# Optimization experiments

Measured on AMD Instinct MI355X. Metric: run time of the kernel, lower is better.

## Reference

```python
import jax, jax.numpy as jnp
import numpy as np

N = 100000   # nodes
E = 1600000  # directed edges
D_IN, D_HID, D_OUT, N_CLS = 128, 256, 128, 10
EPS = 1e-5


def gcn_conv(x, W, b, src, dst, n):
    # PyG GCNConv: h = XW, add self loops, sym-normalize, scatter-add to dst, + bias
    h = x @ W
    loop = jnp.arange(n)
    src_f = jnp.concatenate([src, loop])
    dst_f = jnp.concatenate([dst, loop])
    deg = jax.ops.segment_sum(jnp.ones(src_f.shape[0], h.dtype), dst_f, num_segments=n)
    dinv = jnp.where(deg > 0, jax.lax.rsqrt(deg), jnp.zeros_like(deg))
    norm = dinv[src_f] * dinv[dst_f]                    # [E+N]
    out = jax.ops.segment_sum(h[src_f] * norm[:, None], dst_f, num_segments=n)
    return out + b


def batchnorm(x, gamma, beta):
    # training-mode BatchNorm1d (batch statistics, biased variance)
    mu = x.mean(0)
    var = x.var(0)
    return gamma * (x - mu) * jax.lax.rsqrt(var + EPS) + beta


def setup_inputs() -> dict:
    key = jax.random.key(0)
    ks = jax.random.split(key, 12)
    x = jax.random.normal(ks[0], (N, D_IN), jnp.float32)
    edge_index = jax.random.randint(ks[1], (2, E), 0, N, dtype=jnp.int64)
    def lin(k, fi, fo):
        s = 1.0 / np.sqrt(fi)
        return jax.random.uniform(k, (fi, fo), jnp.float32, -s, s)
    return {
        "x": x, "edge_index": edge_index,
        "W1": lin(ks[2], D_IN, D_HID), "b1": jnp.zeros(D_HID, jnp.float32),
        "g1": jnp.ones(D_HID, jnp.float32), "beta1": jnp.zeros(D_HID, jnp.float32),
        "W2": lin(ks[3], D_HID, D_HID), "b2": jnp.zeros(D_HID, jnp.float32),
        "g2": jnp.ones(D_HID, jnp.float32), "beta2": jnp.zeros(D_HID, jnp.float32),
        "W3": lin(ks[4], D_HID, D_OUT), "b3": jnp.zeros(D_OUT, jnp.float32),
        "g3": jnp.ones(D_OUT, jnp.float32), "beta3": jnp.zeros(D_OUT, jnp.float32),
        "Wout": lin(ks[5], D_OUT, N_CLS), "bout": jnp.zeros(N_CLS, jnp.float32),
    }


def reference(x, edge_index, W1, b1, g1, beta1, W2, b2, g2, beta2,
              W3, b3, g3, beta3, Wout, bout):
    src, dst = edge_index[0], edge_index[1]
    h = jax.nn.relu(batchnorm(gcn_conv(x, W1, b1, src, dst, N), g1, beta1))
    h = jax.nn.relu(batchnorm(gcn_conv(h, W2, b2, src, dst, N), g2, beta2))
    h = jax.nn.relu(batchnorm(gcn_conv(h, W3, b3, src, dst, N), g3, beta3))
    return h @ Wout + bout
```

## Files before the change

kernel.cpp:

```cpp
#include <hip/hip_runtime.h>
#include <hip/hip_fp16.h>
#include <cstdint>
#include <cstddef>

#define EPS_BN 1e-5f
#define NSLICE 16

static inline int cdiv(int a, int b) { return (a + b - 1) / b; }

using half8   = __attribute__((ext_vector_type(8))) _Float16;
using floatx4 = __attribute__((ext_vector_type(4))) float;

__device__ __forceinline__ float atomAddF(float* p, float v) {
    return unsafeAtomicAdd(p, v);
}


__global__ __launch_bounds__(256) void k_hist(const int* __restrict__ dst, int E,
                                              int NBLK, int NBUCK, int* __restrict__ H) {
    __shared__ int h[256];
    int t = threadIdx.x;
    h[t] = 0;
    __syncthreads();
    int base = blockIdx.x * 4096;
#pragma unroll
    for (int j = 0; j < 16; ++j) {
        int e = base + j * 256 + t;
        if (e < E) atomicAdd(&h[dst[e] >> 9], 1);
    }
    __syncthreads();
    if (t < NBUCK) H[t * NBLK + blockIdx.x] = h[t];
}

__global__ __launch_bounds__(256) void k_scan_reduce(const int* __restrict__ in, int m,
                                                     int* __restrict__ bsum) {
    int base = blockIdx.x * 1024;
    int t = threadIdx.x;
    int s = 0;
#pragma unroll
    for (int i = 0; i < 4; ++i) {
        int idx = base + t * 4 + i;
        if (idx < m) s += in[idx];
    }
    __shared__ int sm[256];
    sm[t] = s;
    __syncthreads();
    for (int off = 128; off > 0; off >>= 1) {
        if (t < off) sm[t] += sm[t + off];
        __syncthreads();
    }
    if (t == 0) bsum[blockIdx.x] = sm[0];
}

__global__ void k_scan_bsum(int* __restrict__ bsum, int nb) {
    if (threadIdx.x == 0 && blockIdx.x == 0) {
        int acc = 0;
        for (int i = 0; i < nb; ++i) { int v = bsum[i]; bsum[i] = acc; acc += v; }
    }
}

__global__ __launch_bounds__(256) void k_scan_final(const int* __restrict__ in, int m,
                                                    const int* __restrict__ bsum,
                                                    int* __restrict__ outS) {
    int base = blockIdx.x * 1024;
    int t = threadIdx.x;
    int v[4];
    int s = 0;
#pragma unroll
    for (int i = 0; i < 4; ++i) {
        int idx = base + t * 4 + i;
        v[i] = (idx < m) ? in[idx] : 0;
        s += v[i];
    }
    __shared__ int sm[256];
    sm[t] = s;
    __syncthreads();
    for (int off = 1; off < 256; off <<= 1) {
        int x = (t >= off) ? sm[t - off] : 0;
        __syncthreads();
        sm[t] += x;
        __syncthreads();
    }
    int excl = sm[t] - s + bsum[blockIdx.x];
#pragma unroll
    for (int i = 0; i < 4; ++i) {
        int idx = base + t * 4 + i;
        if (idx < m) { outS[idx] = excl; excl += v[i]; }
    }
}

__global__ __launch_bounds__(256) void k_bucket(const int* __restrict__ src,
                                                const int* __restrict__ dst, int E,
                                                int NBLK, int NBUCK,
                                                const int* __restrict__ S,
                                                unsigned* __restrict__ pairs) {
    __shared__ int cur[256];
    int t = threadIdx.x;
    if (t < NBUCK) cur[t] = S[t * NBLK + blockIdx.x];
    __syncthreads();
    int base = blockIdx.x * 4096;
#pragma unroll
    for (int j = 0; j < 16; ++j) {
        int e = base + j * 256 + t;
        if (e < E) {
            unsigned s = (unsigned)src[e];
            unsigned d = (unsigned)dst[e];
            int p = atomicAdd(&cur[d >> 9], 1);
            pairs[p] = ((d & 511u) << 17) | s;
        }
    }
}

__global__ __launch_bounds__(256) void k_build(const unsigned* __restrict__ pairs,
                                               const int* __restrict__ S,
                                               int NBLK, int NBUCK, int n, int E,
                                               int* __restrict__ endoff,
                                               float* __restrict__ dinv,
                                               int* __restrict__ csr) {
    int b = blockIdx.x;
    int nbase = b << 9;
    int bstart = S[b * NBLK];
    int bend = (b == NBUCK - 1) ? E : S[(b + 1) * NBLK];
    int t = threadIdx.x;
    __shared__ int sdeg[512];
    __shared__ int scur[512];
    __shared__ int stmp[256];
    sdeg[t] = 0; sdeg[t + 256] = 0;
    __syncthreads();
    for (int e = bstart + t; e < bend; e += 256)
        atomicAdd(&sdeg[pairs[e] >> 17], 1);
    __syncthreads();
    int d0 = sdeg[2 * t], d1 = sdeg[2 * t + 1];
    int ps = d0 + d1;
    stmp[t] = ps;
    __syncthreads();
    for (int off = 1; off < 256; off <<= 1) {
        int x = (t >= off) ? stmp[t - off] : 0;
        __syncthreads();
        stmp[t] += x;
        __syncthreads();
    }
    int c0 = bstart + stmp[t] - ps;
    int c1 = c0 + d0;
    scur[2 * t] = c0;
    scur[2 * t + 1] = c1;
    int v0 = nbase + 2 * t, v1 = v0 + 1;
    if (v0 < n) { endoff[v0] = c1;      dinv[v0] = rsqrtf((float)(d0 + 1)); }
    if (v1 < n) { endoff[v1] = c1 + d1; dinv[v1] = rsqrtf((float)(d1 + 1)); }
    __syncthreads();
    for (int e = bstart + t; e < bend; e += 256) {
        unsigned p = pairs[e];
        int pos = atomicAdd(&scur[p >> 17], 1);
        csr[pos] = (int)(p & 0x1FFFFu);
    }
}

__global__ __launch_bounds__(256) void k_prep(const float* __restrict__ x,
                                              const float* __restrict__ dinv,
                                              const float* __restrict__ W1,
                                              const float* __restrict__ W2,
                                              const float* __restrict__ W3,
                                              __half* __restrict__ xh,
                                              __half* __restrict__ Wt1,
                                              __half* __restrict__ Wt2,
                                              __half* __restrict__ Wt3,
                                              float* __restrict__ stats, int n) {
    int idx = blockIdx.x * 256 + threadIdx.x;
    int nx = n * 16;
    if (idx < nx) {
        int row = idx >> 4;
        float dv = dinv[row];
        const float4* p = (const float4*)x + (size_t)idx * 2;
        float4 a = p[0], b = p[1];
        uint4 o; __half2* oh = (__half2*)&o;
        oh[0] = __floats2half2_rn(a.x * dv, a.y * dv);
        oh[1] = __floats2half2_rn(a.z * dv, a.w * dv);
        oh[2] = __floats2half2_rn(b.x * dv, b.y * dv);
        oh[3] = __floats2half2_rn(b.z * dv, b.w * dv);
        ((uint4*)xh)[idx] = o;
        return;
    }
    int r = idx - nx;
    if (r < 32768) {
        int k = r >> 8, c = r & 255;
        Wt1[c * 128 + k] = __float2half(W1[r]);
    } else if (r < 98304) {
        int r2 = r - 32768;
        int k = r2 >> 8, c = r2 & 255;
        Wt2[c * 256 + k] = __float2half(W2[r2]);
    } else if (r < 131072) {
        int r2 = r - 98304;
        int k = r2 >> 7, c = r2 & 127;
        Wt3[c * 256 + k] = __float2half(W3[r2]);
    } else if (r < 131072 + NSLICE * 256 * 6) {
        stats[r - 131072] = 0.f;
    }
}

__device__ __forceinline__ void acc8(float* acc, uint4 d) {
    const __half2* h = (const __half2*)&d;
#pragma unroll
    for (int j = 0; j < 4; ++j) {
        float2 f = __half22float2(h[j]);
        acc[2 * j] += f.x; acc[2 * j + 1] += f.y;
    }
}

template<int D, bool STATS>
__global__ __launch_bounds__(256) void k_gather_h(const int* __restrict__ csr,
                                                  const int* __restrict__ endoff,
                                                  const __half* __restrict__ P,
                                                  const float* __restrict__ dinv,
                                                  __half* __restrict__ S, int n,
                                                  float* __restrict__ sums,
                                                  float* __restrict__ sqs) {
    constexpr int LPN = D / 8;
    constexpr int NPB = 256 / LPN;
    __shared__ float red[STATS ? 2048 : 1];
    int t = threadIdx.x;
    int lane = t % LPN;
    int sub = t / LPN;
    float sacc[8] = {}, sqacc[8] = {};
    for (int vb = blockIdx.x * NPB; vb < n; vb += gridDim.x * NPB) {
        int v = vb + sub;
        if (v >= n) continue;
        int beg = (v == 0) ? 0 : endoff[v - 1];
        int end = endoff[v];
        float acc[8];
        {
            uint4 d = *((const uint4*)(P + (size_t)v * D) + lane);
            const __half2* h = (const __half2*)&d;
#pragma unroll
            for (int j = 0; j < 4; ++j) {
                float2 f = __half22float2(h[j]);
                acc[2 * j] = f.x; acc[2 * j + 1] = f.y;
            }
        }
        int i = beg;
        int rem = (end - beg) & 7;
        if (rem & 4) {
            uint4 dd[4];
#pragma unroll
            for (int u = 0; u < 4; ++u)
                dd[u] = *((const uint4*)(P + (size_t)csr[i + u] * D) + lane);
#pragma unroll
            for (int u = 0; u < 4; ++u) acc8(acc, dd[u]);
            i += 4;
        }
        if (rem & 2) {
            uint4 d0 = *((const uint4*)(P + (size_t)csr[i] * D) + lane);
            uint4 d1 = *((const uint4*)(P + (size_t)csr[i + 1] * D) + lane);
            acc8(acc, d0); acc8(acc, d1);
            i += 2;
        }
        if (rem & 1) {
            uint4 d0 = *((const uint4*)(P + (size_t)csr[i] * D) + lane);
            acc8(acc, d0);
            i += 1;
        }
        if (i < end) {
            uint4 a[8];
#pragma unroll
            for (int u = 0; u < 8; ++u)
                a[u] = *((const uint4*)(P + (size_t)csr[i + u] * D) + lane);
            for (i += 8; i < end; i += 8) {
                uint4 b[8];
#pragma unroll
                for (int u = 0; u < 8; ++u)
                    b[u] = *((const uint4*)(P + (size_t)csr[i + u] * D) + lane);
#pragma unroll
                for (int u = 0; u < 8; ++u) acc8(acc, a[u]);
#pragma unroll
                for (int u = 0; u < 8; ++u) a[u] = b[u];
            }
#pragma unroll
            for (int u = 0; u < 8; ++u) acc8(acc, a[u]);
        }
        float dv = dinv[v];
        uint4 o; __half2* oh = (__half2*)&o;
#pragma unroll
        for (int j = 0; j < 4; ++j) {
            float a0 = acc[2 * j] * dv, a1 = acc[2 * j + 1] * dv;
            oh[j] = __floats2half2_rn(a0, a1);
            if (STATS) {
                sacc[2 * j] += a0;  sqacc[2 * j] += a0 * a0;
                sacc[2 * j + 1] += a1; sqacc[2 * j + 1] += a1 * a1;
            }
        }
        *((uint4*)(S + (size_t)v * D) + lane) = o;
    }
    if (STATS) {
        int slice = blockIdx.x & (NSLICE - 1);
#pragma unroll
        for (int j = 0; j < 8; ++j) red[t * 8 + j] = sacc[j];
        __syncthreads();
        if (t < D) {
            int lc = t >> 3, j = t & 7;
            float ts = 0.f;
#pragma unroll
            for (int s = 0; s < NPB; ++s) ts += red[(s * LPN + lc) * 8 + j];
            atomAddF(&sums[slice * 256 + t], ts);
        }
        __syncthreads();
#pragma unroll
        for (int j = 0; j < 8; ++j) red[t * 8 + j] = sqacc[j];
        __syncthreads();
        if (t < D) {
            int lc = t >> 3, j = t & 7;
            float tq = 0.f;
#pragma unroll
            for (int s = 0; s < NPB; ++s) tq += red[(s * LPN + lc) * 8 + j];
            atomAddF(&sqs[slice * 256 + t], tq);
        }
    }
}

template<int K, int NC, bool SCALE, bool BNIN, bool STATS>
__global__ __launch_bounds__(256) void k_gemm_mfma(const __half* __restrict__ A,
                                                   const __half* __restrict__ Wt,
                                                   const float* __restrict__ dinv,
                                                   const float* __restrict__ isum,
                                                   const float* __restrict__ isq,
                                                   const float* __restrict__ g,
                                                   const float* __restrict__ beta,
                                                   float* __restrict__ osum,
                                                   float* __restrict__ osq,
                                                   __half* __restrict__ C, int n) {
    constexpr int LDA = 40;
    __shared__ _Float16 As[128 * LDA];
    __shared__ _Float16 Bs[128 * LDA];
    __shared__ float ssc[BNIN ? K : 1];
    __shared__ float ssh[BNIN ? K : 1];
    __shared__ float scs[STATS ? 128 : 1];
    __shared__ float scq[STATS ? 128 : 1];
    int tid = threadIdx.x;
    if (BNIN) {
        float nf = (float)n;
        for (int i = tid; i < K; i += 256) {
            float su = 0.f, sq = 0.f;
#pragma unroll
            for (int s = 0; s < NSLICE; ++s) {
                su += isum[s * 256 + i];
                sq += isq[s * 256 + i];
            }
            float mu = su / nf;
            float var = sq / nf - mu * mu;
            float sc = g[i] * rsqrtf(var + EPS_BN);
            ssc[i] = sc; ssh[i] = beta[i] - mu * sc;
        }
        __syncthreads();
    }
    int wave = tid >> 6, lane = tid & 63;
    int wr = wave >> 1, wc = wave & 1;
    int q = lane >> 4, l16 = lane & 15;
    int row0 = blockIdx.x * 128;
    int col0 = blockIdx.y * 128;
    floatx4 acc[4][4];
#pragma unroll
    for (int r = 0; r < 4; ++r)
#pragma unroll
        for (int c = 0; c < 4; ++c) acc[r][c] = (floatx4)0.0f;

    for (int k0 = 0; k0 < K; k0 += 32) {
#pragma unroll
        for (int i = 0; i < 2; ++i) {
            int s = tid + i * 256;
            int r = s >> 2, ks = s & 3;
            uint4 d = *(const uint4*)(A + (size_t)(row0 + r) * K + k0 + ks * 8);
            if (BNIN) {
                const __half2* h = (const __half2*)&d;
                uint4 o; __half2* oh = (__half2*)&o;
                int kb = k0 + ks * 8;
#pragma unroll
                for (int j = 0; j < 4; ++j) {
                    float2 f = __half22float2(h[j]);
                    float y0 = fmaxf(0.f, f.x * ssc[kb + 2 * j]     + ssh[kb + 2 * j]);
                    float y1 = fmaxf(0.f, f.y * ssc[kb + 2 * j + 1] + ssh[kb + 2 * j + 1]);
                    oh[j] = __floats2half2_rn(y0, y1);
                }
                d = o;
            }
            *(uint4*)&As[r * LDA + ks * 8] = d;
        }
#pragma unroll
        for (int i = 0; i < 2; ++i) {
            int s = tid + i * 256;
            int r = s >> 2, ks = s & 3;
            uint4 d = *(const uint4*)(Wt + (size_t)(col0 + r) * K + k0 + ks * 8);
            *(uint4*)&Bs[r * LDA + ks * 8] = d;
        }
        __syncthreads();
        half8 af[4], bf[4];
#pragma unroll
        for (int r = 0; r < 4; ++r)
            af[r] = *(const half8*)&As[(wr * 64 + r * 16 + l16) * LDA + q * 8];
#pragma unroll
        for (int c = 0; c < 4; ++c)
            bf[c] = *(const half8*)&Bs[(wc * 64 + c * 16 + l16) * LDA + q * 8];
#pragma unroll
        for (int r = 0; r < 4; ++r)
#pragma unroll
            for (int c = 0; c < 4; ++c)
                acc[r][c] = __builtin_amdgcn_mfma_f32_16x16x32_f16(af[r], bf[c], acc[r][c], 0, 0, 0);
        __syncthreads();
    }
    float colsum[4] = {};
    float colsq[4]  = {};
#pragma unroll
    for (int r = 0; r < 4; ++r) {
#pragma unroll
        for (int reg = 0; reg < 4; ++reg) {
            int grow = row0 + wr * 64 + r * 16 + q * 4 + reg;
            float sc = 1.f;
            if (SCALE) sc = (grow < n) ? dinv[grow] : 0.f;
            __half* cp = C + (size_t)grow * NC + col0 + wc * 64 + l16;
#pragma unroll
            for (int c = 0; c < 4; ++c) {
                float v = acc[r][c][reg] * sc;
                cp[c * 16] = __float2half(v);
                if (STATS && grow < n) { colsum[c] += v; colsq[c] += v * v; }
            }
        }
    }
    if (STATS) {
        if (tid < 128) { scs[tid] = 0.f; scq[tid] = 0.f; }
        __syncthreads();
#pragma unroll
        for (int c = 0; c < 4; ++c) {
            atomicAdd(&scs[wc * 64 + c * 16 + l16], colsum[c]);
            atomicAdd(&scq[wc * 64 + c * 16 + l16], colsq[c]);
        }
        __syncthreads();
        if (tid < 128) {
            int slice = blockIdx.x & (NSLICE - 1);
            atomAddF(&osum[slice * 256 + col0 + tid], scs[tid]);
            atomAddF(&osq[slice * 256 + col0 + tid], scq[tid]);
        }
    }
}

__global__ __launch_bounds__(256) void k_out(const __half* __restrict__ H,
                                             const float* __restrict__ sums,
                                             const float* __restrict__ sqs,
                                             const float* __restrict__ g,
                                             const float* __restrict__ beta,
                                             const float* __restrict__ Wout,
                                             const float* __restrict__ bout,
                                             float* __restrict__ out, int n) {
    __shared__ float Wl[128 * 10];
    __shared__ float bl[10];
    __shared__ float osc[128];
    __shared__ float osh[128];
    __shared__ float red[256 * 10];
    int tid = threadIdx.x;
    for (int i = tid; i < 1280; i += 256) Wl[i] = Wout[i];
    if (tid < 10) bl[tid] = bout[tid];
    if (tid < 128) {
        float nf = (float)n;
        float su = 0.f, sq = 0.f;
#pragma unroll
        for (int s = 0; s < NSLICE; ++s) {
            su += sums[s * 256 + tid];
            sq += sqs[s * 256 + tid];
        }
        float mu = su / nf;
        float var = sq / nf - mu * mu;
        float sc = g[tid] * rsqrtf(var + EPS_BN);
        osc[tid] = sc; osh[tid] = beta[tid] - mu * sc;
    }
    __syncthreads();
    int rl = tid >> 1;
    int h2 = tid & 1;
    int r = blockIdx.x * 128 + rl;
    float p[10] = {};
    if (r < n) {
        const __half* a = H + (size_t)r * 128 + h2 * 64;
#pragma unroll 8
        for (int k = 0; k < 64; ++k) {
            int col = h2 * 64 + k;
            float av = fmaxf(0.f, __half2float(a[k]) * osc[col] + osh[col]);
            const float* wr = Wl + col * 10;
#pragma unroll
            for (int c = 0; c < 10; ++c) p[c] += av * wr[c];
        }
    }
    float* rr = red + (size_t)tid * 10;
#pragma unroll
    for (int c = 0; c < 10; ++c) rr[c] = p[c];
    __syncthreads();
    if (h2 == 0 && r < n) {
        const float* rb = red + (size_t)tid * 10;
#pragma unroll
        for (int c = 0; c < 10; ++c) {
            out[(size_t)r * 10 + c] = rb[c] + rb[10 + c] + bl[c];
        }
    }
}

extern "C" void kernel_launch(void* const* d_in, const int* in_sizes, int n_in,
                              void* d_out, int out_size, void* d_ws, size_t ws_size,
                              hipStream_t stream) {
    const float* x    = (const float*)d_in[0];
    const int*   ei   = (const int*)d_in[1];
    const float* W1   = (const float*)d_in[2];
    const float* g1   = (const float*)d_in[4];
    const float* be1  = (const float*)d_in[5];
    const float* W2   = (const float*)d_in[6];
    const float* g2   = (const float*)d_in[8];
    const float* be2  = (const float*)d_in[9];
    const float* W3   = (const float*)d_in[10];
    const float* g3   = (const float*)d_in[12];
    const float* be3  = (const float*)d_in[13];
    const float* Wout = (const float*)d_in[14];
    const float* bout = (const float*)d_in[15];
    float* out = (float*)d_out;

    int n = in_sizes[0] / 128;
    int E = in_sizes[1] / 2;
    const int* esrc = ei;
    const int* edst = ei + E;
    int npad = cdiv(n, 128) * 128;
    int NBLK = cdiv(E, 4096);
    int NBUCK = (n + 511) >> 9;
    if (NBUCK > 256) return;
    int m = NBUCK * NBLK;
    int nb2 = cdiv(m, 1024);

    const size_t align = 256;
    auto al = [&](size_t s) { return (s + align - 1) & ~(align - 1); };
    size_t n4 = al((size_t)n * 4 + 512);

    const size_t statsLayer = (size_t)NSLICE * 256 * 2 * 4;
    const size_t statsTotal = statsLayer * 3;

    char* ws = (char*)d_ws;
    size_t o_end   = 0;
    size_t o_dinv  = o_end + n4;
    size_t o_stats = o_dinv + n4;
    size_t o_bsum  = o_stats + statsTotal;
    size_t o_H     = o_bsum + 1024;
    size_t o_Hs    = o_H + al((size_t)m * 4);
    size_t o_csr   = o_Hs + al((size_t)m * 4);
    size_t o_pairs = o_csr + al((size_t)E * 4);
    size_t o_w1    = o_pairs + al((size_t)E * 4);
    size_t o_w2    = o_w1 + al(256 * 128 * 2);
    size_t o_w3    = o_w2 + al(256 * 256 * 2);
    size_t o_A128a = o_w3 + al(128 * 256 * 2);
    size_t o_A128b = o_A128a + al((size_t)npad * 128 * 2);
    size_t o_A256a = o_A128b + al((size_t)npad * 128 * 2);
    size_t o_A256b = o_A256a + al((size_t)npad * 256 * 2);
    size_t need    = o_A256b + (size_t)npad * 256 * 2;
    if (ws_size < need) return;

    int*      endoff = (int*)(ws + o_end);
    float*    dinv   = (float*)(ws + o_dinv);
    float*    stats  = (float*)(ws + o_stats);
    float*    sums1  = stats;
    float*    sqs1   = sums1 + NSLICE * 256;
    float*    sums2  = (float*)(ws + o_stats + statsLayer);
    float*    sqs2   = sums2 + NSLICE * 256;
    float*    sums3  = (float*)(ws + o_stats + 2 * statsLayer);
    float*    sqs3   = sums3 + NSLICE * 256;
    int*      bsum   = (int*)(ws + o_bsum);
    int*      H      = (int*)(ws + o_H);
    int*      Hs     = (int*)(ws + o_Hs);
    int*      csr    = (int*)(ws + o_csr);
    unsigned* pairs  = (unsigned*)(ws + o_pairs);
    __half*   Wt1    = (__half*)(ws + o_w1);
    __half*   Wt2    = (__half*)(ws + o_w2);
    __half*   Wt3    = (__half*)(ws + o_w3);
    __half*   xh     = (__half*)(ws + o_A128a);
    __half*   S3     = (__half*)(ws + o_A128a);
    __half*   G1     = (__half*)(ws + o_A128b);
    __half*   P3     = (__half*)(ws + o_A128b);
    __half*   P1     = (__half*)(ws + o_A256a);
    __half*   S2     = (__half*)(ws + o_A256a);
    __half*   P2     = (__half*)(ws + o_A256b);

    k_hist<<<NBLK, 256, 0, stream>>>(edst, E, NBLK, NBUCK, H);
    k_scan_reduce<<<nb2, 256, 0, stream>>>(H, m, bsum);
    k_scan_bsum<<<1, 64, 0, stream>>>(bsum, nb2);
    k_scan_final<<<nb2, 256, 0, stream>>>(H, m, bsum, Hs);
    k_bucket<<<NBLK, 256, 0, stream>>>(esrc, edst, E, NBLK, NBUCK, Hs, pairs);
    k_build<<<NBUCK, 256, 0, stream>>>(pairs, Hs, NBLK, NBUCK, n, E, endoff, dinv, csr);

    int prepTotal = n * 16 + 131072 + NSLICE * 256 * 6;
    k_prep<<<cdiv(prepTotal, 256), 256, 0, stream>>>(
        x, dinv, W1, W2, W3, xh, Wt1, Wt2, Wt3, stats, n);

    k_gather_h<128, false><<<cdiv(n, 16), 256, 0, stream>>>(
        csr, endoff, xh, dinv, G1, n, nullptr, nullptr);
    k_gemm_mfma<128, 256, false, false, true><<<dim3(npad / 128, 2), 256, 0, stream>>>(
        G1, Wt1, dinv, nullptr, nullptr, nullptr, nullptr, sums1, sqs1, P1, n);

    k_gemm_mfma<256, 256, true, true, false><<<dim3(npad / 128, 2), 256, 0, stream>>>(
        P1, Wt2, dinv, sums1, sqs1, g1, be1, nullptr, nullptr, P2, n);
    k_gather_h<256, true><<<cdiv(n, 8), 256, 0, stream>>>(
        csr, endoff, P2, dinv, S2, n, sums2, sqs2);

    k_gemm_mfma<256, 128, true, true, false><<<dim3(npad / 128, 1), 256, 0, stream>>>(
        S2, Wt3, dinv, sums2, sqs2, g2, be2, nullptr, nullptr, P3, n);
    k_gather_h<128, true><<<cdiv(n, 16), 256, 0, stream>>>(
        csr, endoff, P3, dinv, S3, n, sums3, sqs3);

    k_out<<<cdiv(n, 128), 256, 0, stream>>>(S3, sums3, sqs3, g3, be3, Wout, bout, out, n);
}
```

Measured before the change: 568.5 us.

## Prefetch GEMM tiles into registers and collapse bucket scan into one kernel

The MFMA GEMM now loads the next K-slice of A and W into registers while the current slice is being multiplied, then writes them to shared memory after the compute. This overlaps global load latency with MFMA work. Separately, the three-kernel scan is replaced by a single-block scan, and histogram/bucket blocks now cover 8192 edges each, halving the histogram size. The goal is fewer launches and less preprocessing overhead. The single-block scan serializes more work per thread, and prefetching raises register pressure.

```diff
diff --git a/kernel.cpp b/kernel.cpp
--- a/kernel.cpp
+++ b/kernel.cpp
@@ -22,9 +22,9 @@
     int t = threadIdx.x;
     h[t] = 0;
     __syncthreads();
-    int base = blockIdx.x * 4096;
-#pragma unroll
-    for (int j = 0; j < 16; ++j) {
+    int base = blockIdx.x * 8192;
+#pragma unroll
+    for (int j = 0; j < 32; ++j) {
         int e = base + j * 256 + t;
         if (e < E) atomicAdd(&h[dst[e] >> 9], 1);
     }
@@ -32,47 +32,15 @@
     if (t < NBUCK) H[t * NBLK + blockIdx.x] = h[t];
 }
 
-__global__ __launch_bounds__(256) void k_scan_reduce(const int* __restrict__ in, int m,
-                                                     int* __restrict__ bsum) {
-    int base = blockIdx.x * 1024;
+__global__ __launch_bounds__(256) void k_scan_one(const int* __restrict__ in, int m,
+                                                  int* __restrict__ outS) {
+    __shared__ int sm[256];
     int t = threadIdx.x;
+    int per = (m + 255) / 256;
+    int b0 = t * per;
+    int b1 = b0 + per; if (b1 > m) b1 = m;
     int s = 0;
-#pragma unroll
-    for (int i = 0; i < 4; ++i) {
-        int idx = base + t * 4 + i;
-        if (idx < m) s += in[idx];
-    }
-    __shared__ int sm[256];
-    sm[t] = s;
-    __syncthreads();
-    for (int off = 128; off > 0; off >>= 1) {
-        if (t < off) sm[t] += sm[t + off];
-        __syncthreads();
-    }
-    if (t == 0) bsum[blockIdx.x] = sm[0];
-}
-
-__global__ void k_scan_bsum(int* __restrict__ bsum, int nb) {
-    if (threadIdx.x == 0 && blockIdx.x == 0) {
-        int acc = 0;
-        for (int i = 0; i < nb; ++i) { int v = bsum[i]; bsum[i] = acc; acc += v; }
-    }
-}
-
-__global__ __launch_bounds__(256) void k_scan_final(const int* __restrict__ in, int m,
-                                                    const int* __restrict__ bsum,
-                                                    int* __restrict__ outS) {
-    int base = blockIdx.x * 1024;
-    int t = threadIdx.x;
-    int v[4];
-    int s = 0;
-#pragma unroll
-    for (int i = 0; i < 4; ++i) {
-        int idx = base + t * 4 + i;
-        v[i] = (idx < m) ? in[idx] : 0;
-        s += v[i];
-    }
-    __shared__ int sm[256];
+    for (int i = b0; i < b1; ++i) s += in[i];
     sm[t] = s;
     __syncthreads();
     for (int off = 1; off < 256; off <<= 1) {
@@ -81,12 +49,8 @@
         sm[t] += x;
         __syncthreads();
     }
-    int excl = sm[t] - s + bsum[blockIdx.x];
-#pragma unroll
-    for (int i = 0; i < 4; ++i) {
-        int idx = base + t * 4 + i;
-        if (idx < m) { outS[idx] = excl; excl += v[i]; }
-    }
+    int excl = sm[t] - s;
+    for (int i = b0; i < b1; ++i) { int v = in[i]; outS[i] = excl; excl += v; }
 }
 
 __global__ __launch_bounds__(256) void k_bucket(const int* __restrict__ src,
@@ -98,9 +62,9 @@
     int t = threadIdx.x;
     if (t < NBUCK) cur[t] = S[t * NBLK + blockIdx.x];
     __syncthreads();
-    int base = blockIdx.x * 4096;
-#pragma unroll
-    for (int j = 0; j < 16; ++j) {
+    int base = blockIdx.x * 8192;
+#pragma unroll
+    for (int j = 0; j < 32; ++j) {
         int e = base + j * 256 + t;
         if (e < E) {
             unsigned s = (unsigned)src[e];
@@ -355,22 +319,26 @@
     int q = lane >> 4, l16 = lane & 15;
     int row0 = blockIdx.x * 128;
     int col0 = blockIdx.y * 128;
+    int sr = tid >> 2, sks = tid & 3;
+    const __half* Abase = A + (size_t)(row0 + sr) * K + sks * 8;
+    const __half* Bbase = Wt + (size_t)(col0 + sr) * K + sks * 8;
+    const __half* Abase2 = Abase + 64 * K;
+    const __half* Bbase2 = Bbase + 64 * K;
+
     floatx4 acc[4][4];
 #pragma unroll
     for (int r = 0; r < 4; ++r)
 #pragma unroll
         for (int c = 0; c < 4; ++c) acc[r][c] = (floatx4)0.0f;
 
-    for (int k0 = 0; k0 < K; k0 += 32) {
+    auto storeTiles = [&](uint4* ra, uint4* rb, int kbase) {
 #pragma unroll
         for (int i = 0; i < 2; ++i) {
-            int s = tid + i * 256;
-            int r = s >> 2, ks = s & 3;
-            uint4 d = *(const uint4*)(A + (size_t)(row0 + r) * K + k0 + ks * 8);
+            uint4 d = ra[i];
             if (BNIN) {
                 const __half2* h = (const __half2*)&d;
                 uint4 o; __half2* oh = (__half2*)&o;
-                int kb = k0 + ks * 8;
+                int kb = kbase + sks * 8;
 #pragma unroll
                 for (int j = 0; j < 4; ++j) {
                     float2 f = __half22float2(h[j]);
@@ -380,16 +348,25 @@
                 }
                 d = o;
             }
-            *(uint4*)&As[r * LDA + ks * 8] = d;
-        }
-#pragma unroll
-        for (int i = 0; i < 2; ++i) {
-            int s = tid + i * 256;
-            int r = s >> 2, ks = s & 3;
-            uint4 d = *(const uint4*)(Wt + (size_t)(col0 + r) * K + k0 + ks * 8);
-            *(uint4*)&Bs[r * LDA + ks * 8] = d;
-        }
-        __syncthreads();
+            *(uint4*)&As[(sr + i * 64) * LDA + sks * 8] = d;
+            *(uint4*)&Bs[(sr + i * 64) * LDA + sks * 8] = rb[i];
+        }
+    };
+
+    uint4 ra[2], rb[2];
+    ra[0] = *(const uint4*)(Abase);  ra[1] = *(const uint4*)(Abase2);
+    rb[0] = *(const uint4*)(Bbase);  rb[1] = *(const uint4*)(Bbase2);
+    storeTiles(ra, rb, 0);
+    __syncthreads();
+
+    for (int k0 = 32; k0 <= K; k0 += 32) {
+        bool more = (k0 < K);
+        if (more) {
+            ra[0] = *(const uint4*)(Abase + k0);
+            ra[1] = *(const uint4*)(Abase2 + k0);
+            rb[0] = *(const uint4*)(Bbase + k0);
+            rb[1] = *(const uint4*)(Bbase2 + k0);
+        }
         half8 af[4], bf[4];
 #pragma unroll
         for (int r = 0; r < 4; ++r)
@@ -403,6 +380,10 @@
             for (int c = 0; c < 4; ++c)
                 acc[r][c] = __builtin_amdgcn_mfma_f32_16x16x32_f16(af[r], bf[c], acc[r][c], 0, 0, 0);
         __syncthreads();
+        if (more) {
+            storeTiles(ra, rb, k0);
+            __syncthreads();
+        }
     }
     float colsum[4] = {};
     float colsq[4]  = {};
@@ -520,11 +501,10 @@
     const int* esrc = ei;
     const int* edst = ei + E;
     int npad = cdiv(n, 128) * 128;
-    int NBLK = cdiv(E, 4096);
+    int NBLK = cdiv(E, 8192);
     int NBUCK = (n + 511) >> 9;
     if (NBUCK > 256) return;
     int m = NBUCK * NBLK;
-    int nb2 = cdiv(m, 1024);
 
     const size_t align = 256;
     auto al = [&](size_t s) { return (s + align - 1) & ~(align - 1); };
@@ -537,8 +517,7 @@
     size_t o_end   = 0;
     size_t o_dinv  = o_end + n4;
     size_t o_stats = o_dinv + n4;
-    size_t o_bsum  = o_stats + statsTotal;
-    size_t o_H     = o_bsum + 1024;
+    size_t o_H     = o_stats + statsTotal;
     size_t o_Hs    = o_H + al((size_t)m * 4);
     size_t o_csr   = o_Hs + al((size_t)m * 4);
     size_t o_pairs = o_csr + al((size_t)E * 4);
@@ -561,7 +540,6 @@
     float*    sqs2   = sums2 + NSLICE * 256;
     float*    sums3  = (float*)(ws + o_stats + 2 * statsLayer);
     float*    sqs3   = sums3 + NSLICE * 256;
-    int*      bsum   = (int*)(ws + o_bsum);
     int*      H      = (int*)(ws + o_H);
     int*      Hs     = (int*)(ws + o_Hs);
     int*      csr    = (int*)(ws + o_csr);
@@ -578,9 +556,7 @@
     __half*   P2     = (__half*)(ws + o_A256b);
 
     k_hist<<<NBLK, 256, 0, stream>>>(edst, E, NBLK, NBUCK, H);
-    k_scan_reduce<<<nb2, 256, 0, stream>>>(H, m, bsum);
-    k_scan_bsum<<<1, 64, 0, stream>>>(bsum, nb2);
-    k_scan_final<<<nb2, 256, 0, stream>>>(H, m, bsum, Hs);
+    k_scan_one<<<1, 256, 0, stream>>>(H, m, Hs);
     k_bucket<<<NBLK, 256, 0, stream>>>(esrc, edst, E, NBLK, NBUCK, Hs, pairs);
     k_build<<<NBUCK, 256, 0, stream>>>(pairs, Hs, NBLK, NBUCK, n, E, endoff, dinv, csr);
 
```

After: 646.8 us. 1.14x slower.
